# Kernel tuning notes

Hardware: AMD Instinct MI355X
Metric: run time of the kernel (lower is better)

Reference implementation:

```python
import jax, jax.numpy as jnp
import numpy as np

EPS_DIV = 1e-6    # safe_div clamp
EPS_NORM = 1e-12  # F.normalize eps
EPS_PD = 1e-6     # F.pairwise_distance eps (added to the difference)


def setup_inputs() -> dict:
    key = jax.random.key(0)
    k1, k2, k3 = jax.random.split(key, 3)
    B, N, D, C = 8, 2048, 512, 8192
    x = jax.random.normal(k1, (B, N, D), dtype=jnp.float32)
    W = jax.random.normal(k2, (D, D), dtype=jnp.float32) * (1.0 / np.sqrt(D))
    codebook = jax.random.normal(k3, (C, D), dtype=jnp.float32)
    return {"x": x, "W": W, "codebook": codebook}


def reference(x, W, codebook):
    sg = jax.lax.stop_gradient
    # implicit codebook = Linear(dim, dim, bias=False)(codebook)  -> codebook @ W^T
    imp = codebook @ W.T                                  # [C, D]

    lead = x.shape[:-1]
    D = x.shape[-1]
    xf = x.reshape(-1, D)                                 # [T, D]

    # nearest-neighbor search (no_grad in original): squared-dist argmin == cdist argmin
    d2 = (jnp.sum(xf * xf, axis=-1, keepdims=True)
          - 2.0 * (xf @ imp.T)
          + jnp.sum(imp * imp, axis=-1)[None, :])         # [T, C]
    indices = jnp.argmin(sg(d2), axis=-1)                 # [T]

    qf = imp[indices]                                     # [T, D] gather

    # commit loss: (pairwise_distance(x, q.detach())**2).mean(); torch adds eps to the diff
    diff = xf - sg(qf) + EPS_PD
    commit_loss = jnp.mean(jnp.sum(diff * diff, axis=-1))

    # rotation trick
    norm_x = jnp.linalg.norm(xf, axis=-1, keepdims=True)  # [T, 1]
    norm_q = jnp.linalg.norm(qf, axis=-1, keepdims=True)
    u = xf / jnp.maximum(norm_x, EPS_DIV)
    q = qf / jnp.maximum(norm_q, EPS_DIV)
    s = u + q
    w = sg(s / jnp.maximum(jnp.linalg.norm(s, axis=-1, keepdims=True), EPS_NORM))
    e = xf
    # e - 2 (e.w) w + 2 (e.u_sg) q_sg   (rank-1 products per row)
    rot = (e
           - 2.0 * jnp.sum(e * w, axis=-1, keepdims=True) * w
           + 2.0 * jnp.sum(e * sg(u), axis=-1, keepdims=True) * sg(q))
    quantized = rot * sg(norm_q / jnp.maximum(norm_x, EPS_DIV))

    quantized = quantized.reshape(*lead, D)
    indices = indices.reshape(*lead)
    return quantized, indices, commit_loss
```

## Files before the change

kernel.cpp:

```cpp
#include <hip/hip_runtime.h>
#include <cstdint>
#include <cstddef>

#define DD 512
#define TT 16384
#define CC 8192
#define SPLITC 32
#define EPS_DIV 1e-6f
#define EPS_NORM 1e-12f
#define EPS_PD 1e-6f

typedef _Float16 half8 __attribute__((ext_vector_type(8)));
typedef _Float16 half4 __attribute__((ext_vector_type(4)));
typedef float floatx4 __attribute__((ext_vector_type(4)));

#define GLDS16(g, l) __builtin_amdgcn_global_load_lds( \
    (const __attribute__((address_space(1))) void*)(g), \
    (__attribute__((address_space(3))) void*)(l), 16, 0, 0)

__global__ __launch_bounds__(128) void k_split(const float* __restrict__ src,
                                               _Float16* __restrict__ dst) {
  const int row = blockIdx.x;
  const int col = threadIdx.x * 4;
  float4 v = *(const float4*)(src + (size_t)row * DD + col);
  half4 h, l;
  h.x = (_Float16)v.x; l.x = (_Float16)(v.x - (float)h.x);
  h.y = (_Float16)v.y; l.y = (_Float16)(v.y - (float)h.y);
  h.z = (_Float16)v.z; l.z = (_Float16)(v.z - (float)h.z);
  h.w = (_Float16)v.w; l.w = (_Float16)(v.w - (float)h.w);
  *(half4*)(dst + (size_t)row * 1024 + col) = h;
  *(half4*)(dst + (size_t)row * 1024 + 512 + col) = l;
}

__global__ __launch_bounds__(256) void k_cast_frag(const float* __restrict__ src,
                                                   _Float16* __restrict__ dst) {
  const int rb = blockIdx.x, t = blockIdx.y;
  const int lane = threadIdx.x & 63, s0 = threadIdx.x >> 6;
  const int l15 = lane & 15, quad = lane >> 4;
#pragma unroll
  for (int s = 0; s < 4; ++s) {
    const int slot = s0 * 4 + s;
    const int row = rb * 256 + slot * 16 + l15;
    const float* p = src + (size_t)row * DD + t * 32 + quad * 8;
    float4 v0 = *(const float4*)p;
    float4 v1 = *(const float4*)(p + 4);
    half8 h;
    h[0] = (_Float16)v0.x; h[1] = (_Float16)v0.y;
    h[2] = (_Float16)v0.z; h[3] = (_Float16)v0.w;
    h[4] = (_Float16)v1.x; h[5] = (_Float16)v1.y;
    h[6] = (_Float16)v1.z; h[7] = (_Float16)v1.w;
    *(half8*)(dst + (((size_t)rb * 16 + t) * 16 + slot) * 512 + lane * 8) = h;
  }
}

__global__ __launch_bounds__(256) void k_gemm_mfma(
    const _Float16* __restrict__ cbs, const _Float16* __restrict__ Ws,
    float* __restrict__ imp) {
  __shared__ __align__(16) char smem[65536];
  const int tid = threadIdx.x;
  const int w = tid >> 6, lane = tid & 63;
  const int quad = lane >> 4, l15 = lane & 15;
  const int wm = (w & 1) * 64, wn = (w >> 1) * 64;
  const int c0 = blockIdx.x * 128;
  const int n0 = blockIdx.y * 128;

  const int srow8 = lane >> 3;
  const int scol = ((lane & 7) ^ srow8) << 3;
  size_t arow[4], brow[4];
#pragma unroll
  for (int j = 0; j < 4; ++j) {
    arow[j] = (size_t)(c0 + j * 32 + w * 8 + srow8) * 1024 + scol;
    brow[j] = (size_t)(n0 + j * 32 + w * 8 + srow8) * 1024 + scol;
  }
  int aoff[4], boff[4];
#pragma unroll
  for (int i = 0; i < 4; ++i) {
    aoff[i] = ((wm + i * 16 + l15) * 64 + ((quad ^ (l15 & 7)) << 3)) * 2;
    boff[i] = ((wn + i * 16 + l15) * 64 + ((quad ^ (l15 & 7)) << 3)) * 2;
  }

  auto stage = [&](int buf, int ak, int bk) {
    char* ab = smem + buf * 32768;
    char* bb = ab + 16384;
#pragma unroll
    for (int j = 0; j < 4; ++j) {
      GLDS16(cbs + arow[j] + ak, (_Float16*)ab + (j * 32 + w * 8) * 64);
      GLDS16(Ws  + brow[j] + bk, (_Float16*)bb + (j * 32 + w * 8) * 64);
    }
  };

  floatx4 acc[4][4] = {};
  stage(0, 0, 0);
#pragma unroll 2
  for (int it = 0; it < 24; ++it) {
    __syncthreads();
    if (it < 23) {
      const int n = it + 1;
      const int p = n >> 3, kk = n & 7;
      const int ak = ((p == 2) ? 512 : 0) + kk * 64;
      const int bk = ((p == 1) ? 512 : 0) + kk * 64;
      stage(n & 1, ak, bk);
    }
    const char* ab = smem + (it & 1) * 32768;
    const char* bb = ab + 16384;
#pragma unroll
    for (int ks = 0; ks < 2; ++ks) {
      const int kx = ks * 64;
      half8 a[4], b[4];
#pragma unroll
      for (int mi = 0; mi < 4; ++mi)
        a[mi] = *(const half8*)(ab + (aoff[mi] ^ kx));
#pragma unroll
      for (int ni = 0; ni < 4; ++ni)
        b[ni] = *(const half8*)(bb + (boff[ni] ^ kx));
#pragma unroll
      for (int mi = 0; mi < 4; ++mi)
#pragma unroll
        for (int ni = 0; ni < 4; ++ni)
          acc[mi][ni] = __builtin_amdgcn_mfma_f32_16x16x32_f16(
              a[mi], b[ni], acc[mi][ni], 0, 0, 0);
    }
  }
#pragma unroll
  for (int mi = 0; mi < 4; ++mi)
#pragma unroll
    for (int r = 0; r < 4; ++r) {
      const int c = c0 + wm + mi * 16 + quad * 4 + r;
#pragma unroll
      for (int ni = 0; ni < 4; ++ni) {
        const int d = n0 + wn + ni * 16 + l15;
        imp[(size_t)c * DD + d] = acc[mi][ni][r];
      }
    }
}

__global__ __launch_bounds__(256) void k_row_norm2(
    const float* __restrict__ imp, float* __restrict__ cnorm) {
  const int lane = threadIdx.x & 63;
  const int row = blockIdx.x * 4 + (threadIdx.x >> 6);
  const float* p = imp + (size_t)row * DD + lane * 8;
  float4 a = *(const float4*)p;
  float4 b = *(const float4*)(p + 4);
  float s = a.x * a.x + a.y * a.y + a.z * a.z + a.w * a.w +
            b.x * b.x + b.y * b.y + b.z * b.z + b.w * b.w;
#pragma unroll
  for (int m = 1; m < 64; m <<= 1) s += __shfl_xor(s, m);
  if (lane == 0) cnorm[row] = s;
}

__global__ __launch_bounds__(512, 2) void k_dist_top2(
    const _Float16* __restrict__ xA, const _Float16* __restrict__ ihB,
    const float* __restrict__ cnorm,
    float* __restrict__ bval, int* __restrict__ bidx) {
  __shared__ __align__(16) char smem[131072];
  const int tid = threadIdx.x;
  const int w = tid >> 6, lane = tid & 63;
  const int quad = lane >> 4, l15 = lane & 15;
  const int wr = w >> 2, wc = w & 3;
  const int r0 = blockIdx.x * 256;
  const int c0 = blockIdx.y * 256;

  const _Float16* gA = xA + (size_t)blockIdx.x * 16 * 8192 + w * 1024 + lane * 8;
  const _Float16* gB = ihB + (size_t)blockIdx.y * 16 * 8192 + (wc * 4) * 512 + lane * 8;
  const int ldsDst = w * 2048;
  const int aBase = (wr * 8) * 1024 + lane * 16;

  floatx4 acc[8][4] = {};
  half8 aM[8], bP[4], bQ[4];

#define STAGE_A(T) {                                                           \
    char* d = smem + ((T) & 3) * 16384 + ldsDst;                               \
    const _Float16* g = gA + (size_t)(T) * 8192;                               \
    GLDS16(g, d);                                                              \
    GLDS16(g + 512, d + 1024);                                                 \
  }
#define LOAD_B(BR, T) {                                                        \
    const _Float16* g = gB + (size_t)(T) * 8192;                               \
    _Pragma("unroll")                                                          \
    for (int i = 0; i < 4; ++i) BR[i] = *(const half8*)(g + i * 512);          \
  }

#define CHUNK(T, BCUR, BNXT, DO_B, DO_G, VMC) {                                \
    const char* bb = smem + ((T) & 3) * 16384;                                 \
    _Pragma("unroll")                                                          \
    for (int i = 0; i < 8; ++i)                                                \
      aM[i] = *(const half8*)(bb + aBase + i * 1024);                          \
    if (DO_B) LOAD_B(BNXT, (T) + 1)                                            \
    asm volatile("s_waitcnt vmcnt(" #VMC ")" ::: "memory");                    \
    __builtin_amdgcn_s_barrier();                                              \
    asm volatile("s_waitcnt lgkmcnt(0)" ::: "memory");                         \
    __builtin_amdgcn_sched_barrier(0);                                         \
    if (DO_G) STAGE_A((T) + 3)                                                 \
    __builtin_amdgcn_s_setprio(1);                                             \
    _Pragma("unroll")                                                          \
    for (int mi = 0; mi < 8; ++mi)                                             \
      _Pragma("unroll")                                                        \
      for (int ni = 0; ni < 4; ++ni)                                           \
        acc[mi][ni] = __builtin_amdgcn_mfma_f32_16x16x32_f16(                  \
            aM[mi], BCUR[ni], acc[mi][ni], 0, 0, 0);                           \
    __builtin_amdgcn_s_setprio(0);                                             \
    __builtin_amdgcn_sched_barrier(0);                                         \
  }

  STAGE_A(0) STAGE_A(1) STAGE_A(2)
  LOAD_B(bP, 0)
  asm volatile("s_waitcnt vmcnt(8)" ::: "memory");
  __builtin_amdgcn_s_barrier();
  __builtin_amdgcn_sched_barrier(0);

  CHUNK(0,  bP, bQ, 1, 1, 4)
  CHUNK(1,  bQ, bP, 1, 1, 6)
  CHUNK(2,  bP, bQ, 1, 1, 6)
  CHUNK(3,  bQ, bP, 1, 1, 6)
  CHUNK(4,  bP, bQ, 1, 1, 6)
  CHUNK(5,  bQ, bP, 1, 1, 6)
  CHUNK(6,  bP, bQ, 1, 1, 6)
  CHUNK(7,  bQ, bP, 1, 1, 6)
  CHUNK(8,  bP, bQ, 1, 1, 6)
  CHUNK(9,  bQ, bP, 1, 1, 6)
  CHUNK(10, bP, bQ, 1, 1, 6)
  CHUNK(11, bQ, bP, 1, 1, 6)
  CHUNK(12, bP, bQ, 1, 1, 6)
  CHUNK(13, bQ, bP, 1, 0, 6)
  CHUNK(14, bP, bQ, 1, 0, 4)
  CHUNK(15, bQ, bP, 0, 0, 0)
#undef CHUNK
#undef STAGE_A
#undef LOAD_B

  float cn[4];
#pragma unroll
  for (int ni = 0; ni < 4; ++ni)
    cn[ni] = cnorm[c0 + wc * 64 + ni * 16 + l15];

  __syncthreads();
  float* rv = (float*)smem;
  int* ri = (int*)(smem + 65536);
#pragma unroll
  for (int mi = 0; mi < 8; ++mi)
#pragma unroll
    for (int r = 0; r < 4; ++r) {
      const int row = wr * 128 + mi * 16 + quad * 4 + r;
      float bv = 3.4e38f; int bi = 0x7fffffff;
#pragma unroll
      for (int ni = 0; ni < 4; ++ni) {
        const float v = fmaf(-2.0f, acc[mi][ni][r], cn[ni]);
        const int c = c0 + wc * 64 + ni * 16 + l15;
        if (v < bv) { bv = v; bi = c; }
      }
      const int e = wc * 16 + l15;
      const int g = (row & 31) ^ ((row & 4) << 2);
      const int col = e ^ g;
      rv[row * 64 + col] = bv;
      ri[row * 64 + col] = bi;
    }
  __syncthreads();
  {
    const int row = tid >> 1, h = tid & 1;
    const int g = (row & 31) ^ ((row & 4) << 2);
    float v1 = 3.4e38f, v2 = 3.4e38f;
    int i1 = 0x7fffffff, i2 = 0x7fffffff;
#pragma unroll
    for (int j = 0; j < 32; ++j) {
      const int e = h * 32 + j;
      const int col = e ^ g;
      const float v = rv[row * 64 + col];
      const int i = ri[row * 64 + col];
      if (v < v1 || (v == v1 && i < i1)) { v2 = v1; i2 = i1; v1 = v; i1 = i; }
      else if (v < v2 || (v == v2 && i < i2)) { v2 = v; i2 = i; }
    }
    const float w1 = __shfl_xor(v1, 1), w2 = __shfl_xor(v2, 1);
    const int j1 = __shfl_xor(i1, 1), j2 = __shfl_xor(i2, 1);
    if (w1 < v1 || (w1 == v1 && j1 < i1)) {
      if (v1 < w2 || (v1 == w2 && i1 < j2)) { v2 = v1; i2 = i1; }
      else { v2 = w2; i2 = j2; }
      v1 = w1; i1 = j1;
    } else if (w1 < v2 || (w1 == v2 && j1 < i2)) { v2 = w1; i2 = j1; }
    if (h == 0) {
      const size_t o = ((size_t)blockIdx.y * TT + r0 + row) * 2;
      bval[o] = v1; bval[o + 1] = v2;
      bidx[o] = i1; bidx[o + 1] = i2;
    }
  }
}

__global__ __launch_bounds__(256) void k_epilogue(
    const float* __restrict__ x, const float* __restrict__ imp,
    const float* __restrict__ cnorm,
    const float* __restrict__ bval, const int* __restrict__ bidx,
    float* __restrict__ outq, float* __restrict__ outidx,
    float* __restrict__ rloss) {
  const int lane = threadIdx.x & 63;
  const int row = blockIdx.x * 4 + (threadIdx.x >> 6);
  float v1 = 3.4e38f, v2 = 3.4e38f;
  int i1 = 0x7fffffff, i2 = 0x7fffffff;
  if (lane < SPLITC) {
    const size_t o = ((size_t)lane * TT + row) * 2;
    v1 = bval[o]; v2 = bval[o + 1];
    i1 = bidx[o]; i2 = bidx[o + 1];
  }
#pragma unroll
  for (int m = 1; m < 64; m <<= 1) {
    const float w1 = __shfl_xor(v1, m), w2 = __shfl_xor(v2, m);
    const int j1 = __shfl_xor(i1, m), j2 = __shfl_xor(i2, m);
    if (w1 < v1 || (w1 == v1 && j1 < i1)) {
      if (v1 < w2 || (v1 == w2 && i1 < j2)) { v2 = v1; i2 = i1; }
      else { v2 = w2; i2 = j2; }
      v1 = w1; i1 = j1;
    } else {
      if (w1 < v2 || (w1 == v2 && j1 < i2)) { v2 = w1; i2 = j1; }
    }
  }
  const float* xr = x + (size_t)row * DD + lane * 8;
  float e[8], qa[8], qb[8];
  *(float4*)&e[0] = *(const float4*)xr;
  *(float4*)&e[4] = *(const float4*)(xr + 4);
  const float* q1p = imp + (size_t)i1 * DD + lane * 8;
  const float* q2p = imp + (size_t)i2 * DD + lane * 8;
  *(float4*)&qa[0] = *(const float4*)q1p;
  *(float4*)&qa[4] = *(const float4*)(q1p + 4);
  *(float4*)&qb[0] = *(const float4*)q2p;
  *(float4*)&qb[4] = *(const float4*)(q2p + 4);
  float d1 = 0.f, d2 = 0.f;
#pragma unroll
  for (int k = 0; k < 8; ++k) {
    d1 = fmaf(e[k], qa[k], d1);
    d2 = fmaf(e[k], qb[k], d2);
  }
#pragma unroll
  for (int m = 1; m < 64; m <<= 1) {
    d1 += __shfl_xor(d1, m);
    d2 += __shfl_xor(d2, m);
  }
  const float s1 = fmaf(-2.0f, d1, cnorm[i1]);
  const float s2 = fmaf(-2.0f, d2, cnorm[i2]);
  const bool use2 = (s2 < s1) || (s2 == s1 && i2 < i1);
  const int idx = use2 ? i2 : i1;
  float q[8];
#pragma unroll
  for (int k = 0; k < 8; ++k) q[k] = use2 ? qb[k] : qa[k];

  float xx = 0.f, qq = 0.f, xq = 0.f, cl = 0.f;
#pragma unroll
  for (int k = 0; k < 8; ++k) {
    xx = fmaf(e[k], e[k], xx);
    qq = fmaf(q[k], q[k], qq);
    xq = fmaf(e[k], q[k], xq);
    float d = e[k] - q[k] + EPS_PD;
    cl = fmaf(d, d, cl);
  }
#pragma unroll
  for (int m = 1; m < 64; m <<= 1) {
    xx += __shfl_xor(xx, m);
    qq += __shfl_xor(qq, m);
    xq += __shfl_xor(xq, m);
    cl += __shfl_xor(cl, m);
  }
  const float nx = sqrtf(xx), nq = sqrtf(qq);
  const float dx = fmaxf(nx, EPS_DIV), dq = fmaxf(nq, EPS_DIV);
  const float uu = xx / (dx * dx);
  const float qq2 = qq / (dq * dq);
  const float uq = xq / (dx * dq);
  const float ss = uu + qq2 + 2.0f * uq;
  const float dn = fmaxf(sqrtf(ss), EPS_NORM);
  const float es = xx / dx + xq / dq;
  const float a = 2.0f * es / (dn * dn);
  const float b = 2.0f * (xx / dx);
  const float scale = nq / dx;

  float ov[8];
#pragma unroll
  for (int k = 0; k < 8; ++k) {
    const float qp = q[k] / dq;
    const float sk = e[k] / dx + qp;
    ov[k] = (e[k] - a * sk + b * qp) * scale;
  }
  float* op = outq + (size_t)row * DD + lane * 8;
  *(float4*)op = *(const float4*)&ov[0];
  *(float4*)(op + 4) = *(const float4*)&ov[4];
  if (lane == 0) {
    outidx[row] = (float)idx;
    rloss[row] = cl;
  }
}

__global__ __launch_bounds__(256) void k_loss_final(
    const float* __restrict__ rloss, float* __restrict__ out) {
  __shared__ double red[256];
  const int tid = threadIdx.x;
  double s = 0.0;
  for (int i = tid; i < TT; i += 256) s += (double)rloss[i];
  red[tid] = s;
  __syncthreads();
  for (int st = 128; st > 0; st >>= 1) {
    if (tid < st) red[tid] += red[tid + st];
    __syncthreads();
  }
  if (tid == 0) out[0] = (float)(red[0] / (double)TT);
}

extern "C" void kernel_launch(void* const* d_in, const int* in_sizes, int n_in,
                              void* d_out, int out_size, void* d_ws, size_t ws_size,
                              hipStream_t stream) {
  const float* x  = (const float*)d_in[0];
  const float* W  = (const float*)d_in[1];
  const float* cb = (const float*)d_in[2];
  float* out = (float*)d_out;

  float* imp = (float*)d_ws;
  _Float16* ihB = (_Float16*)(imp + (size_t)CC * DD);
  _Float16* cbs = ihB + (size_t)CC * DD;
  _Float16* xA = cbs;
  _Float16* Ws = cbs + (size_t)CC * 1024;
  float* cnorm = (float*)(Ws + (size_t)DD * 1024);
  float* bval  = cnorm + CC;
  int*   bidx  = (int*)(bval + (size_t)SPLITC * TT * 2);
  float* rloss = (float*)(bidx + (size_t)SPLITC * TT * 2);

  float* out_q    = out;
  float* out_idx  = out + (size_t)TT * DD;
  float* out_loss = out_idx + TT;

  k_split<<<CC, 128, 0, stream>>>(cb, cbs);
  k_split<<<DD, 128, 0, stream>>>(W, Ws);
  k_gemm_mfma<<<dim3(CC / 128, DD / 128), 256, 0, stream>>>(cbs, Ws, imp);
  k_row_norm2<<<CC / 4, 256, 0, stream>>>(imp, cnorm);
  k_cast_frag<<<dim3(CC / 256, 16), 256, 0, stream>>>(imp, ihB);
  k_cast_frag<<<dim3(TT / 256, 16), 256, 0, stream>>>(x, xA);
  k_dist_top2<<<dim3(TT / 256, CC / 256), 512, 0, stream>>>(xA, ihB, cnorm, bval, bidx);
  k_epilogue<<<TT / 4, 256, 0, stream>>>(x, imp, cnorm, bval, bidx, out_q, out_idx, rloss);
  k_loss_final<<<1, 256, 0, stream>>>(rloss, out_loss);
}
```

Before: 328.5 us.

## Shrink distance GEMM tiles to 128x128 with 4 waves and swizzled block order

New measurement: 313.9 us. 4.5% less time.

```diff
diff --git a/kernel.cpp b/kernel.cpp
--- a/kernel.cpp
+++ b/kernel.cpp
@@ -5,7 +5,7 @@
 #define DD 512
 #define TT 16384
 #define CC 8192
-#define SPLITC 32
+#define SPLITC 64
 #define EPS_DIV 1e-6f
 #define EPS_NORM 1e-12f
 #define EPS_PD 1e-6f
@@ -148,28 +148,33 @@
   if (lane == 0) cnorm[row] = s;
 }
 
-__global__ __launch_bounds__(512, 2) void k_dist_top2(
+__global__ __launch_bounds__(256, 3) void k_dist_top2(
     const _Float16* __restrict__ xA, const _Float16* __restrict__ ihB,
     const float* __restrict__ cnorm,
     float* __restrict__ bval, int* __restrict__ bidx) {
-  __shared__ __align__(16) char smem[131072];
+  __shared__ __align__(16) char smem[33792];
   const int tid = threadIdx.x;
   const int w = tid >> 6, lane = tid & 63;
   const int quad = lane >> 4, l15 = lane & 15;
-  const int wr = w >> 2, wc = w & 3;
-  const int r0 = blockIdx.x * 256;
-  const int c0 = blockIdx.y * 256;
-
-  const _Float16* gA = xA + (size_t)blockIdx.x * 16 * 8192 + w * 1024 + lane * 8;
-  const _Float16* gB = ihB + (size_t)blockIdx.y * 16 * 8192 + (wc * 4) * 512 + lane * 8;
+  const int wr = w >> 1, wc = w & 1;
+  const int bid = blockIdx.x;
+  const int bx = (bid & 7) * 16 + ((bid >> 3) & 15);
+  const int by = bid >> 7;
+  const int r0 = bx * 128;
+  const int c0 = by * 128;
+
+  const _Float16* gA = xA + (size_t)(bx >> 1) * 131072 + (bx & 1) * 4096
+                          + w * 1024 + lane * 8;
+  const _Float16* gB = ihB + (size_t)(by >> 1) * 131072 + (by & 1) * 4096
+                          + (wc * 4) * 512 + lane * 8;
   const int ldsDst = w * 2048;
-  const int aBase = (wr * 8) * 1024 + lane * 16;
-
-  floatx4 acc[8][4] = {};
-  half8 aM[8], bP[4], bQ[4];
+  const int aBase = (wr * 4) * 1024 + lane * 16;
+
+  floatx4 acc[4][4] = {};
+  half8 aM[4], bP[4], bQ[4];
 
 #define STAGE_A(T) {                                                           \
-    char* d = smem + ((T) & 3) * 16384 + ldsDst;                               \
+    char* d = smem + ((T) & 3) * 8192 + ldsDst;                                \
     const _Float16* g = gA + (size_t)(T) * 8192;                               \
     GLDS16(g, d);                                                              \
     GLDS16(g + 512, d + 1024);                                                 \
@@ -181,9 +186,9 @@
   }
 
 #define CHUNK(T, BCUR, BNXT, DO_B, DO_G, VMC) {                                \
-    const char* bb = smem + ((T) & 3) * 16384;                                 \
+    const char* bb = smem + ((T) & 3) * 8192;                                  \
     _Pragma("unroll")                                                          \
-    for (int i = 0; i < 8; ++i)                                                \
+    for (int i = 0; i < 4; ++i)                                                \
       aM[i] = *(const half8*)(bb + aBase + i * 1024);                          \
     if (DO_B) LOAD_B(BNXT, (T) + 1)                                            \
     asm volatile("s_waitcnt vmcnt(" #VMC ")" ::: "memory");                    \
@@ -193,7 +198,7 @@
     if (DO_G) STAGE_A((T) + 3)                                                 \
     __builtin_amdgcn_s_setprio(1);                                             \
     _Pragma("unroll")                                                          \
-    for (int mi = 0; mi < 8; ++mi)                                             \
+    for (int mi = 0; mi < 4; ++mi)                                             \
       _Pragma("unroll")                                                        \
       for (int ni = 0; ni < 4; ++ni)                                           \
         acc[mi][ni] = __builtin_amdgcn_mfma_f32_16x16x32_f16(                  \
@@ -235,12 +240,12 @@
 
   __syncthreads();
   float* rv = (float*)smem;
-  int* ri = (int*)(smem + 65536);
-#pragma unroll
-  for (int mi = 0; mi < 8; ++mi)
+  int* ri = (int*)(smem + 16896);
+#pragma unroll
+  for (int mi = 0; mi < 4; ++mi)
 #pragma unroll
     for (int r = 0; r < 4; ++r) {
-      const int row = wr * 128 + mi * 16 + quad * 4 + r;
+      const int row = wr * 64 + mi * 16 + quad * 4 + r;
       float bv = 3.4e38f; int bi = 0x7fffffff;
 #pragma unroll
       for (int ni = 0; ni < 4; ++ni) {
@@ -249,23 +254,19 @@
         if (v < bv) { bv = v; bi = c; }
       }
       const int e = wc * 16 + l15;
-      const int g = (row & 31) ^ ((row & 4) << 2);
-      const int col = e ^ g;
-      rv[row * 64 + col] = bv;
-      ri[row * 64 + col] = bi;
+      rv[row * 33 + e] = bv;
+      ri[row * 33 + e] = bi;
     }
   __syncthreads();
   {
     const int row = tid >> 1, h = tid & 1;
-    const int g = (row & 31) ^ ((row & 4) << 2);
     float v1 = 3.4e38f, v2 = 3.4e38f;
     int i1 = 0x7fffffff, i2 = 0x7fffffff;
 #pragma unroll
-    for (int j = 0; j < 32; ++j) {
-      const int e = h * 32 + j;
-      const int col = e ^ g;
-      const float v = rv[row * 64 + col];
-      const int i = ri[row * 64 + col];
+    for (int j = 0; j < 16; ++j) {
+      const int e = h * 16 + j;
+      const float v = rv[row * 33 + e];
+      const int i = ri[row * 33 + e];
       if (v < v1 || (v == v1 && i < i1)) { v2 = v1; i2 = i1; v1 = v; i1 = i; }
       else if (v < v2 || (v == v2 && i < i2)) { v2 = v; i2 = i; }
     }
@@ -277,7 +278,7 @@
       v1 = w1; i1 = j1;
     } else if (w1 < v2 || (w1 == v2 && j1 < i2)) { v2 = w1; i2 = j1; }
     if (h == 0) {
-      const size_t o = ((size_t)blockIdx.y * TT + r0 + row) * 2;
+      const size_t o = ((size_t)by * TT + r0 + row) * 2;
       bval[o] = v1; bval[o + 1] = v2;
       bidx[o] = i1; bidx[o + 1] = i2;
     }
@@ -292,13 +293,9 @@
     float* __restrict__ rloss) {
   const int lane = threadIdx.x & 63;
   const int row = blockIdx.x * 4 + (threadIdx.x >> 6);
-  float v1 = 3.4e38f, v2 = 3.4e38f;
-  int i1 = 0x7fffffff, i2 = 0x7fffffff;
-  if (lane < SPLITC) {
-    const size_t o = ((size_t)lane * TT + row) * 2;
-    v1 = bval[o]; v2 = bval[o + 1];
-    i1 = bidx[o]; i2 = bidx[o + 1];
-  }
+  const size_t o = ((size_t)lane * TT + row) * 2;
+  float v1 = bval[o], v2 = bval[o + 1];
+  int i1 = bidx[o], i2 = bidx[o + 1];
 #pragma unroll
   for (int m = 1; m < 64; m <<= 1) {
     const float w1 = __shfl_xor(v1, m), w2 = __shfl_xor(v2, m);
@@ -427,7 +424,7 @@
   k_row_norm2<<<CC / 4, 256, 0, stream>>>(imp, cnorm);
   k_cast_frag<<<dim3(CC / 256, 16), 256, 0, stream>>>(imp, ihB);
   k_cast_frag<<<dim3(TT / 256, 16), 256, 0, stream>>>(x, xA);
-  k_dist_top2<<<dim3(TT / 256, CC / 256), 512, 0, stream>>>(xA, ihB, cnorm, bval, bidx);
+  k_dist_top2<<<(TT / 128) * (CC / 128), 256, 0, stream>>>(xA, ihB, cnorm, bval, bidx);
   k_epilogue<<<TT / 4, 256, 0, stream>>>(x, imp, cnorm, bval, bidx, out_q, out_idx, rloss);
   k_loss_final<<<1, 256, 0, stream>>>(rloss, out_loss);
 }
```
